# Optimization experiments

Measured on AMD Instinct MI355X. Metric: run time of the kernel, lower is better.

## Reference

```python
import jax, jax.numpy as jnp
import numpy as np


def _conv(x, w, b, stride, pad):
    # x: [N,C,H,W], w: [O,I,kh,kw]
    y = jax.lax.conv_general_dilated(
        x, w, (stride, stride), [(pad, pad), (pad, pad)],
        dimension_numbers=('NCHW', 'OIHW', 'NCHW'))
    return y + b[None, :, None, None]


def _block(x, w1, b1, w2, b2, stride):
    # BasicBlock with BN folded: conv3x3 -> relu -> conv3x3
    h = jax.nn.relu(_conv(x, w1, b1, stride, 1))
    return _conv(h, w2, b2, 1, 1)


def setup_inputs() -> dict:
    key = jax.random.key(0)
    keys = iter(jax.random.split(key, 64))

    def rn(shape):
        fan_in = int(np.prod(shape[1:])) if len(shape) > 1 else shape[0]
        return jax.random.normal(next(keys), shape, jnp.float32) * (1.0 / np.sqrt(fan_in))

    d = {}
    d['inputs'] = jax.random.normal(next(keys), (128, 3, 64, 64), jnp.float32)
    d['probs'] = jax.random.uniform(next(keys), (128, 15), jnp.float32)
    d['seed_w'] = rn((64, 3, 3, 3))
    d['seed_b'] = jnp.zeros((64,), jnp.float32)
    specs = [(64, 64), (64, 128), (128, 256)]  # (cin, cout) per group
    for g, (ci, co) in enumerate(specs):
        d[f'g{g}_ds_w'] = rn((co, ci, 1, 1))
        d[f'g{g}_ds_b'] = jnp.zeros((co,), jnp.float32)
        d[f'g{g}_b0_w1'] = rn((co, ci, 3, 3))
        d[f'g{g}_b0_b1'] = jnp.zeros((co,), jnp.float32)
        d[f'g{g}_b0_w2'] = rn((co, co, 3, 3))
        d[f'g{g}_b0_b2'] = jnp.zeros((co,), jnp.float32)
        d[f'g{g}_r_w1'] = rn((4, co, co, 3, 3))
        d[f'g{g}_r_b1'] = jnp.zeros((4, co), jnp.float32)
        d[f'g{g}_r_w2'] = rn((4, co, co, 3, 3))
        d[f'g{g}_r_b2'] = jnp.zeros((4, co), jnp.float32)
    d['fc_w'] = rn((1000, 256))
    d['fc_b'] = jnp.zeros((1000,), jnp.float32)
    return d


def reference(inputs, probs, seed_w, seed_b,
              g0_ds_w, g0_ds_b, g0_b0_w1, g0_b0_b1, g0_b0_w2, g0_b0_b2,
              g0_r_w1, g0_r_b1, g0_r_w2, g0_r_b2,
              g1_ds_w, g1_ds_b, g1_b0_w1, g1_b0_b1, g1_b0_w2, g1_b0_b2,
              g1_r_w1, g1_r_b1, g1_r_w2, g1_r_b2,
              g2_ds_w, g2_ds_b, g2_b0_w1, g2_b0_b1, g2_b0_w2, g2_b0_b2,
              g2_r_w1, g2_r_b1, g2_r_w2, g2_r_b2,
              fc_w, fc_b):
    # policy[k, n] in {0,1}: hard-threshold of agent probs at 0.5 (forward_real)
    policy = jnp.where(probs < 0.5, 0.0, 1.0).astype(inputs.dtype).T  # [15, B]
    x = jax.nn.relu(_conv(inputs, seed_w, seed_b, 1, 1))
    groups = [
        (g0_ds_w, g0_ds_b, g0_b0_w1, g0_b0_b1, g0_b0_w2, g0_b0_b2, g0_r_w1, g0_r_b1, g0_r_w2, g0_r_b2, 1),
        (g1_ds_w, g1_ds_b, g1_b0_w1, g1_b0_b1, g1_b0_w2, g1_b0_b2, g1_r_w1, g1_r_b1, g1_r_w2, g1_r_b2, 2),
        (g2_ds_w, g2_ds_b, g2_b0_w1, g2_b0_b1, g2_b0_w2, g2_b0_b2, g2_r_w1, g2_r_b1, g2_r_w2, g2_r_b2, 2),
    ]
    idx = 0
    for (ds_w, ds_b, b0_w1, b0_b1, b0_w2, b0_b2, r_w1, r_b1, r_w2, r_b2, s) in groups:
        # first block of the group: strided, with 1x1 downsample residual
        residual = _conv(x, ds_w, ds_b, s, 0)
        fx = _block(x, b0_w1, b0_b1, b0_w2, b0_b2, s)
        m = policy[idx][:, None, None, None]
        idx += 1
        x = m * jax.nn.relu(residual + fx) + (1.0 - m) * residual
        # remaining 4 identity-residual blocks
        for j in range(4):
            residual = x
            fx = _block(x, r_w1[j], r_b1[j], r_w2[j], r_b2[j], 1)
            m = policy[idx][:, None, None, None]
            idx += 1
            x = m * jax.nn.relu(residual + fx) + (1.0 - m) * residual
    pooled = x.mean(axis=(2, 3))  # global average pool [B, 256]
    return pooled @ fc_w.T + fc_b
```

## Files before the change

### kernel.cpp

```cpp
#include <hip/hip_runtime.h>

using bf = unsigned short;
typedef __attribute__((ext_vector_type(8))) short short8v;
typedef __attribute__((ext_vector_type(4))) float f32x4;
typedef __attribute__((ext_vector_type(4))) unsigned int u32x4;
typedef __attribute__((ext_vector_type(2))) unsigned int u32x2;

__device__ __forceinline__ float bf2f(bf u) { return __uint_as_float(((unsigned)u) << 16); }
__device__ __forceinline__ bf f2bf(float f) {
    unsigned x = __float_as_uint(f);
    x += 0x7fffu + ((x >> 16) & 1u);
    return (bf)(x >> 16);
}

__device__ __forceinline__ void gload16(const bf* g, bf* l) {
    __builtin_amdgcn_global_load_lds(
        (const __attribute__((address_space(1))) void*)g,
        (__attribute__((address_space(3))) void*)l, 16, 0, 0);
}

template <int CI, int CC, int RS, int STRIDE, bool RELU, int CMB, int TH, int TW, int W>
__global__ __launch_bounds__(256, 3) void conv_mfma(
    const bf* __restrict__ X, const bf* __restrict__ Wp,
    const float* __restrict__ bias, bf* __restrict__ Y,
    const bf* __restrict__ res, const float* __restrict__ probs,
    const bf* __restrict__ zpage, int kidx, int Co) {
    constexpr int PAD = (RS == 3) ? 1 : 0;
    constexpr int IN_ROWS = (TH - 1) * STRIDE + RS;
    constexpr int IN_COLS = (TW - 1) * STRIDE + RS;
    constexpr int NG = CC / 8;
    constexpr int HIN = W * STRIDE;
    constexpr int RSRS = RS * RS;
    constexpr int NCH = CI / CC;
    constexpr bool DIRECT = (RS == 1);
    constexpr int TG = IN_ROWS * IN_COLS * NG;
    constexpr int NITER = (TG + 255) / 256;
    constexpr int NPX = TH * TW;
    constexpr int NF = NPX / 32;
    constexpr int TPR = W / TW;
    constexpr int KSH = (STRIDE == 2) ? 1 : 0;

    __shared__ bf sX[DIRECT ? 8 : IN_ROWS * IN_COLS * CC];

    const int tid = threadIdx.x;
    const int n = blockIdx.z;
    const int coBase = blockIdx.y << 6;
    const int bx = blockIdx.x;
    const int tr0 = (bx / TPR) * TH;
    const int tc0 = (bx % TPR) * TW;

    bool active = true;
    if (kidx >= 0) active = (probs[n * 15 + kidx] >= 0.5f);
    if (!active) return;

    const int lane = tid & 63;
    const int wid = tid >> 6;
    const int l15 = lane & 15;
    const int lq = lane >> 4;
    const int wm = wid >> 1;
    const int wn = wid & 1;

    f32x4 acc[2][NF] = {};
    int prow[NF], pcol[NF];
#pragma unroll
    for (int nf = 0; nf < NF; ++nf) {
        int p = wn * (NPX / 2) + nf * 16 + l15;
        prow[nf] = p / TW;
        pcol[nf] = p % TW;
    }

    const bf* Xn = X + (size_t)n * HIN * HIN * CI;

    if constexpr (DIRECT) {
#pragma unroll
        for (int ch = 0; ch < NCH; ++ch) {
#pragma unroll
            for (int kk = 0; kk < CC / 32; ++kk) {
                short8v a[2], b[NF];
#pragma unroll
                for (int mf = 0; mf < 2; ++mf) {
                    int co = coBase + wm * 32 + mf * 16 + l15;
                    a[mf] = *reinterpret_cast<const short8v*>(
                        Wp + ((size_t)ch * Co + co) * CC + kk * 32 + lq * 8);
                }
#pragma unroll
                for (int nf = 0; nf < NF; ++nf) {
                    b[nf] = *reinterpret_cast<const short8v*>(
                        Xn + ((size_t)((tr0 + prow[nf]) * STRIDE) * HIN +
                              (tc0 + pcol[nf]) * STRIDE) * CI + ch * CC + kk * 32 + lq * 8);
                }
#pragma unroll
                for (int mf = 0; mf < 2; ++mf)
#pragma unroll
                    for (int nf = 0; nf < NF; ++nf)
                        acc[mf][nf] = __builtin_amdgcn_mfma_f32_16x16x32_bf16(
                            a[mf], b[nf], acc[mf][nf], 0, 0, 0);
            }
        }
    } else {
        for (int ch = 0; ch < NCH; ++ch) {
            if (ch) __syncthreads();
#pragma unroll
            for (int i = 0; i < NITER; ++i) {
                int g = tid + i * 256;
                if (TG % 256 == 0 || g < TG) {
                    int ir = g / (IN_COLS * NG);
                    int rem = g - ir * (IN_COLS * NG);
                    int ic = rem / NG;
                    int gc = rem - ic * NG;
                    int in_r = tr0 * STRIDE - PAD + ir;
                    int in_c = tc0 * STRIDE - PAD + ic;
                    int gsrc = gc ^ ((ic >> KSH) & (NG - 1));
                    const bf* src = zpage;
                    if ((unsigned)in_r < (unsigned)HIN && (unsigned)in_c < (unsigned)HIN)
                        src = Xn + ((size_t)in_r * HIN + in_c) * CI + ch * CC + gsrc * 8;
                    gload16(src, &sX[(size_t)g * 8]);
                }
            }
            __syncthreads();

            if constexpr (CC >= 32) {
#pragma unroll
                for (int j = 0; j < RSRS; ++j) {
                    const int dh = j / RS;
                    const int dw = j % RS;
#pragma unroll
                    for (int kk = 0; kk < CC / 32; ++kk) {
                        short8v a[2], b[NF];
#pragma unroll
                        for (int mf = 0; mf < 2; ++mf) {
                            int co = coBase + wm * 32 + mf * 16 + l15;
                            a[mf] = *reinterpret_cast<const short8v*>(
                                Wp + (((size_t)(ch * RSRS + j) * Co + co) * CC + kk * 32 + lq * 8));
                        }
#pragma unroll
                        for (int nf = 0; nf < NF; ++nf) {
                            int ir = prow[nf] * STRIDE + dh;
                            int ic = pcol[nf] * STRIDE + dw;
                            int gk = (kk * 4 + lq) ^ ((ic >> KSH) & (NG - 1));
                            b[nf] = *reinterpret_cast<const short8v*>(
                                &sX[((ir * IN_COLS + ic) * NG + gk) * 8]);
                        }
#pragma unroll
                        for (int mf = 0; mf < 2; ++mf)
#pragma unroll
                            for (int nf = 0; nf < NF; ++nf)
                                acc[mf][nf] = __builtin_amdgcn_mfma_f32_16x16x32_bf16(
                                    a[mf], b[nf], acc[mf][nf], 0, 0, 0);
                    }
                }
            } else {
#pragma unroll
                for (int kt = 0; kt < 3; ++kt) {
                    int j = kt * 4 + lq;
                    int jj = (j < 9) ? j : 0;
                    int dh = jj / 3, dw = jj % 3;
                    short8v a[2], b[NF];
#pragma unroll
                    for (int mf = 0; mf < 2; ++mf) {
                        int co = coBase + wm * 32 + mf * 16 + l15;
                        a[mf] = *reinterpret_cast<const short8v*>(Wp + ((size_t)j * Co + co) * 8);
                    }
#pragma unroll
                    for (int nf = 0; nf < NF; ++nf) {
                        int ir = prow[nf] + dh;
                        int ic = pcol[nf] + dw;
                        b[nf] = *reinterpret_cast<const short8v*>(&sX[(ir * IN_COLS + ic) * 8]);
                    }
#pragma unroll
                    for (int mf = 0; mf < 2; ++mf)
#pragma unroll
                        for (int nf = 0; nf < NF; ++nf)
                            acc[mf][nf] = __builtin_amdgcn_mfma_f32_16x16x32_bf16(
                                a[mf], b[nf], acc[mf][nf], 0, 0, 0);
                }
            }
        }
    }

#pragma unroll
    for (int mf = 0; mf < 2; ++mf) {
        int co0 = coBase + wm * 32 + mf * 16 + lq * 4;
        float4 b4 = *reinterpret_cast<const float4*>(bias + co0);
        float bb[4] = {b4.x, b4.y, b4.z, b4.w};
#pragma unroll
        for (int nf = 0; nf < NF; ++nf) {
            size_t off = ((size_t)n * W * W + (size_t)(tr0 + prow[nf]) * W + tc0 + pcol[nf]) * Co + co0;
            float v[4];
#pragma unroll
            for (int i = 0; i < 4; ++i) v[i] = acc[mf][nf][i] + bb[i];
            if constexpr (CMB >= 1) {
                u32x2 r2 = *reinterpret_cast<const u32x2*>(res + off);
                bf rr[4] = {(bf)(r2[0] & 0xffff), (bf)(r2[0] >> 16),
                            (bf)(r2[1] & 0xffff), (bf)(r2[1] >> 16)};
#pragma unroll
                for (int i = 0; i < 4; ++i) v[i] = fmaxf(v[i] + bf2f(rr[i]), 0.f);
            }
            if constexpr (RELU) {
#pragma unroll
                for (int i = 0; i < 4; ++i) v[i] = fmaxf(v[i], 0.f);
            }
            unsigned lo = (unsigned)f2bf(v[0]) | ((unsigned)f2bf(v[1]) << 16);
            unsigned hi = (unsigned)f2bf(v[2]) | ((unsigned)f2bf(v[3]) << 16);
            u32x2 o2 = {lo, hi};
            *reinterpret_cast<u32x2*>(Y + off) = o2;
        }
    }
}

#define NSEG 34
struct Seg {
    const float* src;
    bf* dst;
    int Co, Ci, RSRS, CC, JPAD, blk0;
};
struct SegArgs {
    Seg s[NSEG];
};
__global__ void repack_all(SegArgs A) {
    int b = blockIdx.x;
    int lo = 0;
#pragma unroll 1
    for (int i = 1; i < NSEG; ++i)
        if (A.s[i].blk0 <= b) lo = i;
    Seg sg = A.s[lo];
    int NCH_ = (sg.Ci + sg.CC - 1) / sg.CC;
    size_t total8 = ((size_t)NCH_ * sg.JPAD * sg.Co * sg.CC) >> 3;
    size_t i8 = (size_t)(b - sg.blk0) * 256 + threadIdx.x;
    if (i8 >= total8) return;
    size_t e = i8 * 8;
    int cw = (int)(e % sg.CC);
    int co = (int)((e / sg.CC) % sg.Co);
    int j = (int)((e / ((size_t)sg.CC * sg.Co)) % sg.JPAD);
    int ch = (int)(e / ((size_t)sg.CC * sg.Co * sg.JPAD));
    bf tmp[8];
#pragma unroll
    for (int k = 0; k < 8; ++k) {
        int ci = ch * sg.CC + cw + k;
        float v = 0.f;
        if (ci < sg.Ci && j < sg.RSRS) v = sg.src[((size_t)co * sg.Ci + ci) * sg.RSRS + j];
        tmp[k] = f2bf(v);
    }
    u32x4 o;
#pragma unroll
    for (int k = 0; k < 4; ++k) o[k] = (unsigned)tmp[2 * k] | ((unsigned)tmp[2 * k + 1] << 16);
    *reinterpret_cast<u32x4*>(sg.dst + e) = o;
}

__global__ void cvt_in(const float* __restrict__ in, bf* __restrict__ out) {
    size_t idx = (size_t)blockIdx.x * 256 + threadIdx.x;
    int c = (int)(idx & 7);
    size_t pix = idx >> 3;
    int w = (int)(pix & 63);
    int h = (int)((pix >> 6) & 63);
    int n = (int)(pix >> 12);
    float v = 0.f;
    if (c < 3) v = in[(((size_t)n * 3 + c) * 64 + h) * 64 + w];
    out[idx] = f2bf(v);
}

__global__ void zero_k(bf* p) {
    u32x4 z = {0, 0, 0, 0};
    *reinterpret_cast<u32x4*>(p + (size_t)threadIdx.x * 8) = z;
}

__global__ void pool_k(const bf* __restrict__ X, float* __restrict__ pooled) {
    __shared__ float red[8][256];
    int n = blockIdx.x;
    int g = threadIdx.x & 31;
    int slice = threadIdx.x >> 5;
    float acc[8] = {};
    for (int p = slice * 32; p < slice * 32 + 32; ++p) {
        u32x4 v = *reinterpret_cast<const u32x4*>(X + ((size_t)n * 256 + p) * 256 + g * 8);
#pragma unroll
        for (int i = 0; i < 4; ++i) {
            acc[2 * i] += bf2f((bf)(v[i] & 0xffff));
            acc[2 * i + 1] += bf2f((bf)(v[i] >> 16));
        }
    }
#pragma unroll
    for (int i = 0; i < 8; ++i) red[slice][g * 8 + i] = acc[i];
    __syncthreads();
    if (slice == 0) {
#pragma unroll
        for (int i = 0; i < 8; ++i) {
            float s = 0.f;
#pragma unroll
            for (int ss = 0; ss < 8; ++ss) s += red[ss][g * 8 + i];
            pooled[n * 256 + g * 8 + i] = s * (1.f / 256.f);
        }
    }
}

__global__ void fc_k(const float* __restrict__ pooled, const float* __restrict__ fw,
                     const float* __restrict__ fb, float* __restrict__ out) {
    __shared__ float sp[256];
    int n = blockIdx.x;
    sp[threadIdx.x] = pooled[n * 256 + threadIdx.x];
    __syncthreads();
    for (int o = threadIdx.x; o < 1000; o += 256) {
        float acc = fb[o];
        for (int k = 0; k < 256; ++k) acc += sp[k] * fw[(size_t)o * 256 + k];
        out[(size_t)n * 1000 + o] = acc;
    }
}

template <int CIN, int COUT, int S, int TH, int TW, int W, int CC1>
static void run_group(hipStream_t st, bf* X, bf* H, bf* OUT, const bf* zp,
                      bf* wp_ds, const float* ds_b, bf* wp_w1, const float* b1,
                      bf* wp_w2, const float* b2, bf* const* wp_rw1, const float* rb1,
                      bf* const* wp_rw2, const float* rb2, const float* probs_c,
                      int kbase, int NB) {
    dim3 grid((W / TH) * (W / TW), COUT / 64, NB);
    conv_mfma<CIN, 64, 1, S, false, 0, TH, TW, W><<<grid, 256, 0, st>>>(
        X, wp_ds, ds_b, OUT, nullptr, nullptr, zp, -1, COUT);
    conv_mfma<CIN, CC1, 3, S, true, 0, TH, TW, W><<<grid, 256, 0, st>>>(
        X, wp_w1, b1, H, nullptr, probs_c, zp, kbase, COUT);
    conv_mfma<COUT, 64, 3, 1, false, 2, TH, TW, W><<<grid, 256, 0, st>>>(
        H, wp_w2, b2, OUT, OUT, probs_c, zp, kbase, COUT);
    for (int j = 0; j < 4; ++j) {
        conv_mfma<COUT, 64, 3, 1, true, 0, TH, TW, W><<<grid, 256, 0, st>>>(
            OUT, wp_rw1[j], rb1 + j * COUT, H, nullptr, probs_c, zp, kbase + 1 + j, COUT);
        conv_mfma<COUT, 64, 3, 1, false, 2, TH, TW, W><<<grid, 256, 0, st>>>(
            H, wp_rw2[j], rb2 + j * COUT, OUT, OUT, probs_c, zp, kbase + 1 + j, COUT);
    }
}

extern "C" void kernel_launch(void* const* d_in, const int* in_sizes, int n_in,
                              void* d_out, int out_size, void* d_ws, size_t ws_size,
                              hipStream_t stream) {
    (void)in_sizes; (void)n_in; (void)out_size;
    const float* input = (const float*)d_in[0];
    const float* probs = (const float*)d_in[1];
    const float* seed_w = (const float*)d_in[2];
    const float* seed_b = (const float*)d_in[3];
    const float* fc_w = (const float*)d_in[34];
    const float* fc_b = (const float*)d_in[35];

    char* pw = (char*)d_ws;
    auto alloc = [&](size_t bytes) -> void* {
        void* r = (void*)pw;
        pw += ((bytes + 255) & ~(size_t)255);
        return r;
    };

    bf* xin = (bf*)alloc(128ull * 64 * 64 * 8 * 2);
    float* pooled = (float*)alloc(128 * 256 * 4);
    bf* zpage = (bf*)alloc(256);

    SegArgs sa;
    int nseg = 0;
    int blkAcc = 0;
    auto pack = [&](const float* w, int Co_, int Ci_, int RSRS_, int CC_, int JPAD_) -> bf* {
        int NCH_ = (Ci_ + CC_ - 1) / CC_;
        size_t total = (size_t)NCH_ * JPAD_ * Co_ * CC_;
        bf* wp = (bf*)alloc(total * 2);
        sa.s[nseg] = {w, wp, Co_, Ci_, RSRS_, CC_, JPAD_, blkAcc};
        blkAcc += (int)(((total >> 3) + 255) / 256);
        ++nseg;
        return wp;
    };

    zero_k<<<dim3(1), 16, 0, stream>>>(zpage);
    cvt_in<<<dim3(16384), 256, 0, stream>>>(input, xin);

    bf* wpSeed = pack(seed_w, 64, 3, 9, 8, 12);
    const int cis[3] = {64, 64, 128};
    const int cos[3] = {64, 128, 256};
    const int cc1s[3] = {64, 32, 32};
    bf* wp_ds[3];
    bf* wp_w1[3];
    bf* wp_w2[3];
    bf* wp_rw1[3][4];
    bf* wp_rw2[3][4];
    const float *ds_b[3], *b1[3], *b2[3], *rb1[3], *rb2[3];
    for (int g = 0; g < 3; ++g) {
        int base = 4 + g * 10;
        const float* dsw = (const float*)d_in[base + 0];
        ds_b[g] = (const float*)d_in[base + 1];
        const float* w1 = (const float*)d_in[base + 2];
        b1[g] = (const float*)d_in[base + 3];
        const float* w2 = (const float*)d_in[base + 4];
        b2[g] = (const float*)d_in[base + 5];
        const float* rw1 = (const float*)d_in[base + 6];
        rb1[g] = (const float*)d_in[base + 7];
        const float* rw2 = (const float*)d_in[base + 8];
        rb2[g] = (const float*)d_in[base + 9];
        int Ci = cis[g], Co = cos[g];
        wp_ds[g] = pack(dsw, Co, Ci, 1, 64, 1);
        wp_w1[g] = pack(w1, Co, Ci, 9, cc1s[g], 9);
        wp_w2[g] = pack(w2, Co, Co, 9, 64, 9);
        for (int j = 0; j < 4; ++j) {
            wp_rw1[g][j] = pack(rw1 + (size_t)j * Co * Co * 9, Co, Co, 9, 64, 9);
            wp_rw2[g][j] = pack(rw2 + (size_t)j * Co * Co * 9, Co, Co, 9, 64, 9);
        }
    }
    for (int i = nseg; i < NSEG; ++i) sa.s[i] = {nullptr, nullptr, 1, 1, 1, 1, 1, 0x7fffffff};
    repack_all<<<dim3(blkAcc), 256, 0, stream>>>(sa);

    size_t used = (size_t)(pw - (char*)d_ws);
    size_t avail = (ws_size > used) ? (ws_size - used) : 0;
    const size_t PER_IMG = 64ull * 64 * 64 * 2;
    int NB = 128;
    while (NB > 8 && (size_t)3 * NB * PER_IMG + 4096 > avail) NB >>= 1;

    bf* A = (bf*)alloc((size_t)NB * PER_IMG);
    bf* Bb = (bf*)alloc((size_t)NB * PER_IMG);
    bf* C = (bf*)alloc((size_t)NB * PER_IMG);

    for (int n0 = 0; n0 < 128; n0 += NB) {
        const float* pc = probs + (size_t)n0 * 15;
        conv_mfma<8, 8, 3, 1, true, 0, 8, 16, 64><<<dim3(32, 1, NB), 256, 0, stream>>>(
            xin + (size_t)n0 * 64 * 64 * 8, wpSeed, seed_b, A, nullptr, nullptr, zpage, -1, 64);

        run_group<64, 64, 1, 8, 16, 64, 64>(stream, A, Bb, C, zpage,
                                            wp_ds[0], ds_b[0], wp_w1[0], b1[0],
                                            wp_w2[0], b2[0], wp_rw1[0], rb1[0],
                                            wp_rw2[0], rb2[0], pc, 0, NB);
        run_group<64, 128, 2, 8, 16, 32, 32>(stream, C, Bb, A, zpage,
                                             wp_ds[1], ds_b[1], wp_w1[1], b1[1],
                                             wp_w2[1], b2[1], wp_rw1[1], rb1[1],
                                             wp_rw2[1], rb2[1], pc, 5, NB);
        run_group<128, 256, 2, 8, 8, 16, 32>(stream, A, Bb, C, zpage,
                                             wp_ds[2], ds_b[2], wp_w1[2], b1[2],
                                             wp_w2[2], b2[2], wp_rw1[2], rb1[2],
                                             wp_rw2[2], rb2[2], pc, 10, NB);

        pool_k<<<dim3(NB), 256, 0, stream>>>(C, pooled + (size_t)n0 * 256);
    }

    fc_k<<<dim3(128), 256, 0, stream>>>(pooled, fc_w, fc_b, (float*)d_out);
}
```

Baseline: 2.360 ms.

## Double-buffer LDS staging with 32-channel chunks and register-held weights

Switches all 3x3 convs to 32-channel input chunks and double-buffers the LDS tile, so the next chunk's global-to-LDS copy overlaps the MFMA compute on the current one. All nine taps of weights for a chunk are preloaded into registers before use. Tile shapes are also split per conv type: first-block convs and residual convs get separate tile sizes, and group 2 switches to larger tiles. This adds register pressure (18 short8v for weights) and more LDS, which may reduce occupancy under launch_bounds(256,3).

```diff
diff --git a/kernel.cpp b/kernel.cpp
--- a/kernel.cpp
+++ b/kernel.cpp
@@ -35,12 +35,15 @@
     constexpr bool DIRECT = (RS == 1);
     constexpr int TG = IN_ROWS * IN_COLS * NG;
     constexpr int NITER = (TG + 255) / 256;
+    constexpr int TGP = NITER * 256;
+    constexpr int BUFE = TGP * 8;
     constexpr int NPX = TH * TW;
     constexpr int NF = NPX / 32;
     constexpr int TPR = W / TW;
     constexpr int KSH = (STRIDE == 2) ? 1 : 0;
-
-    __shared__ bf sX[DIRECT ? 8 : IN_ROWS * IN_COLS * CC];
+    constexpr bool PIPE = (!DIRECT) && (CC == 32) && (NCH > 1);
+
+    __shared__ bf sX[DIRECT ? 8 : (PIPE ? 2 * BUFE : BUFE)];
 
     const int tid = threadIdx.x;
     const int n = blockIdx.z;
@@ -97,84 +100,116 @@
                             a[mf], b[nf], acc[mf][nf], 0, 0, 0);
             }
         }
-    } else {
-        for (int ch = 0; ch < NCH; ++ch) {
-            if (ch) __syncthreads();
+    } else if constexpr (CC == 32) {
+        short8v wl[RSRS][2];
+
+        auto wload = [&](int ch) {
+#pragma unroll
+            for (int j = 0; j < RSRS; ++j)
+#pragma unroll
+                for (int mf = 0; mf < 2; ++mf) {
+                    int co = coBase + wm * 32 + mf * 16 + l15;
+                    wl[j][mf] = *reinterpret_cast<const short8v*>(
+                        Wp + (((size_t)(ch * RSRS + j) * Co + co) * CC + lq * 8));
+                }
+        };
+
+        auto stage = [&](int ch, bf* buf) {
 #pragma unroll
             for (int i = 0; i < NITER; ++i) {
                 int g = tid + i * 256;
-                if (TG % 256 == 0 || g < TG) {
-                    int ir = g / (IN_COLS * NG);
-                    int rem = g - ir * (IN_COLS * NG);
-                    int ic = rem / NG;
-                    int gc = rem - ic * NG;
-                    int in_r = tr0 * STRIDE - PAD + ir;
-                    int in_c = tc0 * STRIDE - PAD + ic;
-                    int gsrc = gc ^ ((ic >> KSH) & (NG - 1));
-                    const bf* src = zpage;
-                    if ((unsigned)in_r < (unsigned)HIN && (unsigned)in_c < (unsigned)HIN)
-                        src = Xn + ((size_t)in_r * HIN + in_c) * CI + ch * CC + gsrc * 8;
-                    gload16(src, &sX[(size_t)g * 8]);
+                int ir = g / (IN_COLS * NG);
+                int rem = g - ir * (IN_COLS * NG);
+                int ic = rem / NG;
+                int gc = rem - ic * NG;
+                int in_r = tr0 * STRIDE - PAD + ir;
+                int in_c = tc0 * STRIDE - PAD + ic;
+                int gsrc = gc ^ ((ic >> KSH) & (NG - 1));
+                const bf* src = zpage;
+                if (g < TG && (unsigned)in_r < (unsigned)HIN && (unsigned)in_c < (unsigned)HIN)
+                    src = Xn + ((size_t)in_r * HIN + in_c) * CI + ch * CC + gsrc * 8;
+                gload16(src, &buf[(size_t)g * 8]);
+            }
+        };
+
+        auto compute = [&](const bf* buf) {
+#pragma unroll
+            for (int j = 0; j < RSRS; ++j) {
+                const int dh = j / RS;
+                const int dw = j % RS;
+                short8v b[NF];
+#pragma unroll
+                for (int nf = 0; nf < NF; ++nf) {
+                    int ir = prow[nf] * STRIDE + dh;
+                    int ic = pcol[nf] * STRIDE + dw;
+                    int gk = lq ^ ((ic >> KSH) & (NG - 1));
+                    b[nf] = *reinterpret_cast<const short8v*>(
+                        &buf[((ir * IN_COLS + ic) * NG + gk) * 8]);
                 }
-            }
-            __syncthreads();
-
-            if constexpr (CC >= 32) {
-#pragma unroll
-                for (int j = 0; j < RSRS; ++j) {
-                    const int dh = j / RS;
-                    const int dw = j % RS;
-#pragma unroll
-                    for (int kk = 0; kk < CC / 32; ++kk) {
-                        short8v a[2], b[NF];
-#pragma unroll
-                        for (int mf = 0; mf < 2; ++mf) {
-                            int co = coBase + wm * 32 + mf * 16 + l15;
-                            a[mf] = *reinterpret_cast<const short8v*>(
-                                Wp + (((size_t)(ch * RSRS + j) * Co + co) * CC + kk * 32 + lq * 8));
-                        }
-#pragma unroll
-                        for (int nf = 0; nf < NF; ++nf) {
-                            int ir = prow[nf] * STRIDE + dh;
-                            int ic = pcol[nf] * STRIDE + dw;
-                            int gk = (kk * 4 + lq) ^ ((ic >> KSH) & (NG - 1));
-                            b[nf] = *reinterpret_cast<const short8v*>(
-                                &sX[((ir * IN_COLS + ic) * NG + gk) * 8]);
-                        }
-#pragma unroll
-                        for (int mf = 0; mf < 2; ++mf)
-#pragma unroll
-                            for (int nf = 0; nf < NF; ++nf)
-                                acc[mf][nf] = __builtin_amdgcn_mfma_f32_16x16x32_bf16(
-                                    a[mf], b[nf], acc[mf][nf], 0, 0, 0);
-                    }
-                }
-            } else {
-#pragma unroll
-                for (int kt = 0; kt < 3; ++kt) {
-                    int j = kt * 4 + lq;
-                    int jj = (j < 9) ? j : 0;
-                    int dh = jj / 3, dw = jj % 3;
-                    short8v a[2], b[NF];
-#pragma unroll
-                    for (int mf = 0; mf < 2; ++mf) {
-                        int co = coBase + wm * 32 + mf * 16 + l15;
-                        a[mf] = *reinterpret_cast<const short8v*>(Wp + ((size_t)j * Co + co) * 8);
-                    }
-#pragma unroll
-                    for (int nf = 0; nf < NF; ++nf) {
-                        int ir = prow[nf] + dh;
-                        int ic = pcol[nf] + dw;
-                        b[nf] = *reinterpret_cast<const short8v*>(&sX[(ir * IN_COLS + ic) * 8]);
-                    }
-#pragma unroll
-                    for (int mf = 0; mf < 2; ++mf)
-#pragma unroll
-                        for (int nf = 0; nf < NF; ++nf)
-                            acc[mf][nf] = __builtin_amdgcn_mfma_f32_16x16x32_bf16(
-                                a[mf], b[nf], acc[mf][nf], 0, 0, 0);
-                }
-            }
+#pragma unroll
+                for (int mf = 0; mf < 2; ++mf)
+#pragma unroll
+                    for (int nf = 0; nf < NF; ++nf)
+                        acc[mf][nf] = __builtin_amdgcn_mfma_f32_16x16x32_bf16(
+                            wl[j][mf], b[nf], acc[mf][nf], 0, 0, 0);
+            }
+        };
+
+        wload(0);
+        __builtin_amdgcn_sched_barrier(0);
+        stage(0, sX);
+        __syncthreads();
+#pragma unroll 1
+        for (int ch = 0; ch < NCH; ++ch) {
+            const bf* cur = sX + (size_t)(PIPE ? (ch & 1) : 0) * BUFE;
+            bf* nxt = sX + (size_t)(PIPE ? ((ch + 1) & 1) : 0) * BUFE;
+            if (ch + 1 < NCH) stage(ch + 1, nxt);
+            __builtin_amdgcn_sched_barrier(0);
+            compute(cur);
+            if (ch + 1 < NCH) {
+                wload(ch + 1);
+                __syncthreads();
+            }
+        }
+    } else {
+        stage_seed:;
+#pragma unroll
+        for (int i = 0; i < NITER; ++i) {
+            int g = tid + i * 256;
+            int ir = g / (IN_COLS * NG);
+            int rem = g - ir * (IN_COLS * NG);
+            int ic = rem / NG;
+            int in_r = tr0 - PAD + ir;
+            int in_c = tc0 - PAD + ic;
+            const bf* src = zpage;
+            if (g < TG && (unsigned)in_r < (unsigned)HIN && (unsigned)in_c < (unsigned)HIN)
+                src = Xn + ((size_t)in_r * HIN + in_c) * CI;
+            gload16(src, &sX[(size_t)g * 8]);
+        }
+        __syncthreads();
+#pragma unroll
+        for (int kt = 0; kt < 3; ++kt) {
+            int j = kt * 4 + lq;
+            int jj = (j < 9) ? j : 0;
+            int dh = jj / 3, dw = jj % 3;
+            short8v a[2], b[NF];
+#pragma unroll
+            for (int mf = 0; mf < 2; ++mf) {
+                int co = coBase + wm * 32 + mf * 16 + l15;
+                a[mf] = *reinterpret_cast<const short8v*>(Wp + ((size_t)j * Co + co) * 8);
+            }
+#pragma unroll
+            for (int nf = 0; nf < NF; ++nf) {
+                int ir = prow[nf] + dh;
+                int ic = pcol[nf] + dw;
+                b[nf] = *reinterpret_cast<const short8v*>(&sX[(ir * IN_COLS + ic) * 8]);
+            }
+#pragma unroll
+            for (int mf = 0; mf < 2; ++mf)
+#pragma unroll
+                for (int nf = 0; nf < NF; ++nf)
+                    acc[mf][nf] = __builtin_amdgcn_mfma_f32_16x16x32_bf16(
+                        a[mf], b[nf], acc[mf][nf], 0, 0, 0);
         }
     }
 
@@ -305,23 +340,24 @@
     }
 }
 
-template <int CIN, int COUT, int S, int TH, int TW, int W, int CC1>
+template <int CIN, int COUT, int S, int TH1, int TW1, int TH2, int TW2, int W>
 static void run_group(hipStream_t st, bf* X, bf* H, bf* OUT, const bf* zp,
                       bf* wp_ds, const float* ds_b, bf* wp_w1, const float* b1,
                       bf* wp_w2, const float* b2, bf* const* wp_rw1, const float* rb1,
                       bf* const* wp_rw2, const float* rb2, const float* probs_c,
                       int kbase, int NB) {
-    dim3 grid((W / TH) * (W / TW), COUT / 64, NB);
-    conv_mfma<CIN, 64, 1, S, false, 0, TH, TW, W><<<grid, 256, 0, st>>>(
+    dim3 grid1((W / TH1) * (W / TW1), COUT / 64, NB);
+    dim3 grid2((W / TH2) * (W / TW2), COUT / 64, NB);
+    conv_mfma<CIN, 64, 1, S, false, 0, TH2, TW2, W><<<grid2, 256, 0, st>>>(
         X, wp_ds, ds_b, OUT, nullptr, nullptr, zp, -1, COUT);
-    conv_mfma<CIN, CC1, 3, S, true, 0, TH, TW, W><<<grid, 256, 0, st>>>(
+    conv_mfma<CIN, 32, 3, S, true, 0, TH2, TW2, W><<<grid2, 256, 0, st>>>(
         X, wp_w1, b1, H, nullptr, probs_c, zp, kbase, COUT);
-    conv_mfma<COUT, 64, 3, 1, false, 2, TH, TW, W><<<grid, 256, 0, st>>>(
+    conv_mfma<COUT, 32, 3, 1, false, 2, TH1, TW1, W><<<grid1, 256, 0, st>>>(
         H, wp_w2, b2, OUT, OUT, probs_c, zp, kbase, COUT);
     for (int j = 0; j < 4; ++j) {
-        conv_mfma<COUT, 64, 3, 1, true, 0, TH, TW, W><<<grid, 256, 0, st>>>(
+        conv_mfma<COUT, 32, 3, 1, true, 0, TH1, TW1, W><<<grid1, 256, 0, st>>>(
             OUT, wp_rw1[j], rb1 + j * COUT, H, nullptr, probs_c, zp, kbase + 1 + j, COUT);
-        conv_mfma<COUT, 64, 3, 1, false, 2, TH, TW, W><<<grid, 256, 0, st>>>(
+        conv_mfma<COUT, 32, 3, 1, false, 2, TH1, TW1, W><<<grid1, 256, 0, st>>>(
             H, wp_rw2[j], rb2 + j * COUT, OUT, OUT, probs_c, zp, kbase + 1 + j, COUT);
     }
 }
@@ -367,7 +403,6 @@
     bf* wpSeed = pack(seed_w, 64, 3, 9, 8, 12);
     const int cis[3] = {64, 64, 128};
     const int cos[3] = {64, 128, 256};
-    const int cc1s[3] = {64, 32, 32};
     bf* wp_ds[3];
     bf* wp_w1[3];
     bf* wp_w2[3];
@@ -388,11 +423,11 @@
         rb2[g] = (const float*)d_in[base + 9];
         int Ci = cis[g], Co = cos[g];
         wp_ds[g] = pack(dsw, Co, Ci, 1, 64, 1);
-        wp_w1[g] = pack(w1, Co, Ci, 9, cc1s[g], 9);
-        wp_w2[g] = pack(w2, Co, Co, 9, 64, 9);
+        wp_w1[g] = pack(w1, Co, Ci, 9, 32, 9);
+        wp_w2[g] = pack(w2, Co, Co, 9, 32, 9);
         for (int j = 0; j < 4; ++j) {
-            wp_rw1[g][j] = pack(rw1 + (size_t)j * Co * Co * 9, Co, Co, 9, 64, 9);
-            wp_rw2[g][j] = pack(rw2 + (size_t)j * Co * Co * 9, Co, Co, 9, 64, 9);
+            wp_rw1[g][j] = pack(rw1 + (size_t)j * Co * Co * 9, Co, Co, 9, 32, 9);
+            wp_rw2[g][j] = pack(rw2 + (size_t)j * Co * Co * 9, Co, Co, 9, 32, 9);
         }
     }
     for (int i = nseg; i < NSEG; ++i) sa.s[i] = {nullptr, nullptr, 1, 1, 1, 1, 1, 0x7fffffff};
@@ -413,18 +448,18 @@
         conv_mfma<8, 8, 3, 1, true, 0, 8, 16, 64><<<dim3(32, 1, NB), 256, 0, stream>>>(
             xin + (size_t)n0 * 64 * 64 * 8, wpSeed, seed_b, A, nullptr, nullptr, zpage, -1, 64);
 
-        run_group<64, 64, 1, 8, 16, 64, 64>(stream, A, Bb, C, zpage,
-                                            wp_ds[0], ds_b[0], wp_w1[0], b1[0],
-                                            wp_w2[0], b2[0], wp_rw1[0], rb1[0],
-                                            wp_rw2[0], rb2[0], pc, 0, NB);
-        run_group<64, 128, 2, 8, 16, 32, 32>(stream, C, Bb, A, zpage,
-                                             wp_ds[1], ds_b[1], wp_w1[1], b1[1],
-                                             wp_w2[1], b2[1], wp_rw1[1], rb1[1],
-                                             wp_rw2[1], rb2[1], pc, 5, NB);
-        run_group<128, 256, 2, 8, 8, 16, 32>(stream, A, Bb, C, zpage,
-                                             wp_ds[2], ds_b[2], wp_w1[2], b1[2],
-                                             wp_w2[2], b2[2], wp_rw1[2], rb1[2],
-                                             wp_rw2[2], rb2[2], pc, 10, NB);
+        run_group<64, 64, 1, 8, 16, 8, 16, 64>(stream, A, Bb, C, zpage,
+                                               wp_ds[0], ds_b[0], wp_w1[0], b1[0],
+                                               wp_w2[0], b2[0], wp_rw1[0], rb1[0],
+                                               wp_rw2[0], rb2[0], pc, 0, NB);
+        run_group<64, 128, 2, 8, 16, 8, 8, 32>(stream, C, Bb, A, zpage,
+                                               wp_ds[1], ds_b[1], wp_w1[1], b1[1],
+                                               wp_w2[1], b2[1], wp_rw1[1], rb1[1],
+                                               wp_rw2[1], rb2[1], pc, 5, NB);
+        run_group<128, 256, 2, 8, 16, 8, 8, 16>(stream, A, Bb, C, zpage,
+                                                wp_ds[2], ds_b[2], wp_w1[2], b1[2],
+                                                wp_w2[2], b2[2], wp_rw1[2], rb1[2],
+                                                wp_rw2[2], rb2[2], pc, 10, NB);
 
         pool_k<<<dim3(NB), 256, 0, stream>>>(C, pooled + (size_t)n0 * 256);
     }
```

Result: slower. 3.096 ms (+31.2%).

## Fuse downsample 1x1 conv into first block conv, seed input cast, and pool+fc

Applied to the files above, without the earlier changes.

The 1x1 strided downsample conv is now computed inside the first 3x3 conv of each group, reusing the staged input tile (the center tap). Inactive images run only the downsample path. The fp32-to-bf16 input conversion kernel is folded into the seed conv's tile load, and average pooling is merged with the FC layer. This removes separate launches and redundant reads of activations, at the cost of extra registers for a second accumulator set in the fused kernel.

```diff
diff --git a/kernel.cpp b/kernel.cpp
--- a/kernel.cpp
+++ b/kernel.cpp
@@ -19,28 +19,27 @@
         (__attribute__((address_space(3))) void*)l, 16, 0, 0);
 }
 
-template <int CI, int CC, int RS, int STRIDE, bool RELU, int CMB, int TH, int TW, int W>
+template <int CI, int CC, int STRIDE, bool SEED, bool DS, bool RELU, int CMB,
+          int TH, int TW, int W>
 __global__ __launch_bounds__(256, 3) void conv_mfma(
-    const bf* __restrict__ X, const bf* __restrict__ Wp,
-    const float* __restrict__ bias, bf* __restrict__ Y,
+    const bf* __restrict__ X, const float* __restrict__ Xf,
+    const bf* __restrict__ Wp, const bf* __restrict__ Wds,
+    const float* __restrict__ bias, const float* __restrict__ dsb,
+    bf* __restrict__ Y, bf* __restrict__ Yds,
     const bf* __restrict__ res, const float* __restrict__ probs,
     const bf* __restrict__ zpage, int kidx, int Co) {
-    constexpr int PAD = (RS == 3) ? 1 : 0;
-    constexpr int IN_ROWS = (TH - 1) * STRIDE + RS;
-    constexpr int IN_COLS = (TW - 1) * STRIDE + RS;
+    constexpr int IN_ROWS = (TH - 1) * STRIDE + 3;
+    constexpr int IN_COLS = (TW - 1) * STRIDE + 3;
     constexpr int NG = CC / 8;
     constexpr int HIN = W * STRIDE;
-    constexpr int RSRS = RS * RS;
     constexpr int NCH = CI / CC;
-    constexpr bool DIRECT = (RS == 1);
     constexpr int TG = IN_ROWS * IN_COLS * NG;
     constexpr int NITER = (TG + 255) / 256;
-    constexpr int NPX = TH * TW;
-    constexpr int NF = NPX / 32;
+    constexpr int NF = (TH * TW) / 32;
     constexpr int TPR = W / TW;
     constexpr int KSH = (STRIDE == 2) ? 1 : 0;
 
-    __shared__ bf sX[DIRECT ? 8 : IN_ROWS * IN_COLS * CC];
+    __shared__ bf sX[SEED ? TG * 8 : NITER * 256 * 8];
 
     const int tid = threadIdx.x;
     const int n = blockIdx.z;
@@ -51,7 +50,7 @@
 
     bool active = true;
     if (kidx >= 0) active = (probs[n * 15 + kidx] >= 0.5f);
-    if (!active) return;
+    if (!active && !DS) return;
 
     const int lane = tid & 63;
     const int wid = tid >> 6;
@@ -61,33 +60,70 @@
     const int wn = wid & 1;
 
     f32x4 acc[2][NF] = {};
+    f32x4 accds[DS ? 2 : 1][DS ? NF : 1] = {};
     int prow[NF], pcol[NF];
 #pragma unroll
     for (int nf = 0; nf < NF; ++nf) {
-        int p = wn * (NPX / 2) + nf * 16 + l15;
+        int p = wn * (TH * TW / 2) + nf * 16 + l15;
         prow[nf] = p / TW;
         pcol[nf] = p % TW;
     }
 
     const bf* Xn = X + (size_t)n * HIN * HIN * CI;
 
-    if constexpr (DIRECT) {
-#pragma unroll
-        for (int ch = 0; ch < NCH; ++ch) {
-#pragma unroll
-            for (int kk = 0; kk < CC / 32; ++kk) {
+    for (int ch = 0; ch < NCH; ++ch) {
+        if (ch) __syncthreads();
+        if constexpr (SEED) {
+            const float* Xfn = Xf + (size_t)n * 3 * HIN * HIN;
+            if (tid < TG) {
+                int ir = tid / IN_COLS;
+                int ic = tid % IN_COLS;
+                int in_r = tr0 - 1 + ir;
+                int in_c = tc0 - 1 + ic;
+                u32x4 u = {0, 0, 0, 0};
+                if ((unsigned)in_r < (unsigned)HIN && (unsigned)in_c < (unsigned)HIN) {
+                    const float* p = Xfn + (size_t)in_r * HIN + in_c;
+                    u[0] = (unsigned)f2bf(p[0]) | ((unsigned)f2bf(p[HIN * HIN]) << 16);
+                    u[1] = (unsigned)f2bf(p[2 * HIN * HIN]);
+                }
+                *reinterpret_cast<u32x4*>(&sX[(size_t)tid * 8]) = u;
+            }
+        } else {
+#pragma unroll
+            for (int i = 0; i < NITER; ++i) {
+                int g = tid + i * 256;
+                int ir = g / (IN_COLS * NG);
+                int rem = g - ir * (IN_COLS * NG);
+                int ic = rem / NG;
+                int gc = rem - ic * NG;
+                int in_r = tr0 * STRIDE - 1 + ir;
+                int in_c = tc0 * STRIDE - 1 + ic;
+                int gsrc = gc ^ ((ic >> KSH) & (NG - 1));
+                const bf* src = zpage;
+                if (g < TG && (unsigned)in_r < (unsigned)HIN && (unsigned)in_c < (unsigned)HIN)
+                    src = Xn + ((size_t)in_r * HIN + in_c) * CI + ch * CC + gsrc * 8;
+                gload16(src, &sX[(size_t)g * 8]);
+            }
+        }
+        __syncthreads();
+
+        if constexpr (SEED) {
+#pragma unroll
+            for (int kt = 0; kt < 3; ++kt) {
+                int j = kt * 4 + lq;
+                int jj = (j < 9) ? j : 0;
+                int dh = jj / 3, dw = jj % 3;
                 short8v a[2], b[NF];
 #pragma unroll
                 for (int mf = 0; mf < 2; ++mf) {
                     int co = coBase + wm * 32 + mf * 16 + l15;
-                    a[mf] = *reinterpret_cast<const short8v*>(
-                        Wp + ((size_t)ch * Co + co) * CC + kk * 32 + lq * 8);
+                    a[mf] = *reinterpret_cast<const short8v*>(Wp + ((size_t)j * Co + co) * 8);
                 }
 #pragma unroll
                 for (int nf = 0; nf < NF; ++nf) {
-                    b[nf] = *reinterpret_cast<const short8v*>(
-                        Xn + ((size_t)((tr0 + prow[nf]) * STRIDE) * HIN +
-                              (tc0 + pcol[nf]) * STRIDE) * CI + ch * CC + kk * 32 + lq * 8);
+                    int ir = prow[nf] + dh;
+                    int ic = pcol[nf] + dw;
+                    b[nf] = *reinterpret_cast<const short8v*>(&sX[(ir * IN_COLS + ic) * 8]);
                 }
 #pragma unroll
                 for (int mf = 0; mf < 2; ++mf)
@@ -96,76 +132,27 @@
                         acc[mf][nf] = __builtin_amdgcn_mfma_f32_16x16x32_bf16(
                             a[mf], b[nf], acc[mf][nf], 0, 0, 0);
             }
-        }
-    } else {
-        for (int ch = 0; ch < NCH; ++ch) {
-            if (ch) __syncthreads();
-#pragma unroll
-            for (int i = 0; i < NITER; ++i) {
-                int g = tid + i * 256;
-                if (TG % 256 == 0 || g < TG) {
-                    int ir = g / (IN_COLS * NG);
-                    int rem = g - ir * (IN_COLS * NG);
-                    int ic = rem / NG;
-                    int gc = rem - ic * NG;
-                    int in_r = tr0 * STRIDE - PAD + ir;
-                    int in_c = tc0 * STRIDE - PAD + ic;
-                    int gsrc = gc ^ ((ic >> KSH) & (NG - 1));
-                    const bf* src = zpage;
-                    if ((unsigned)in_r < (unsigned)HIN && (unsigned)in_c < (unsigned)HIN)
-                        src = Xn + ((size_t)in_r * HIN + in_c) * CI + ch * CC + gsrc * 8;
-                    gload16(src, &sX[(size_t)g * 8]);
-                }
-            }
-            __syncthreads();
-
-            if constexpr (CC >= 32) {
-#pragma unroll
-                for (int j = 0; j < RSRS; ++j) {
-                    const int dh = j / RS;
-                    const int dw = j % RS;
-#pragma unroll
-                    for (int kk = 0; kk < CC / 32; ++kk) {
-                        short8v a[2], b[NF];
-#pragma unroll
-                        for (int mf = 0; mf < 2; ++mf) {
-                            int co = coBase + wm * 32 + mf * 16 + l15;
-                            a[mf] = *reinterpret_cast<const short8v*>(
-                                Wp + (((size_t)(ch * RSRS + j) * Co + co) * CC + kk * 32 + lq * 8));
-                        }
-#pragma unroll
-                        for (int nf = 0; nf < NF; ++nf) {
-                            int ir = prow[nf] * STRIDE + dh;
-                            int ic = pcol[nf] * STRIDE + dw;
-                            int gk = (kk * 4 + lq) ^ ((ic >> KSH) & (NG - 1));
-                            b[nf] = *reinterpret_cast<const short8v*>(
-                                &sX[((ir * IN_COLS + ic) * NG + gk) * 8]);
-                        }
-#pragma unroll
-                        for (int mf = 0; mf < 2; ++mf)
-#pragma unroll
-                            for (int nf = 0; nf < NF; ++nf)
-                                acc[mf][nf] = __builtin_amdgcn_mfma_f32_16x16x32_bf16(
-                                    a[mf], b[nf], acc[mf][nf], 0, 0, 0);
-                    }
-                }
-            } else {
-#pragma unroll
-                for (int kt = 0; kt < 3; ++kt) {
-                    int j = kt * 4 + lq;
-                    int jj = (j < 9) ? j : 0;
-                    int dh = jj / 3, dw = jj % 3;
+        } else if (active) {
+#pragma unroll
+            for (int j = 0; j < 9; ++j) {
+                const int dh = j / 3;
+                const int dw = j % 3;
+#pragma unroll
+                for (int kk = 0; kk < CC / 32; ++kk) {
                     short8v a[2], b[NF];
 #pragma unroll
                     for (int mf = 0; mf < 2; ++mf) {
                         int co = coBase + wm * 32 + mf * 16 + l15;
-                        a[mf] = *reinterpret_cast<const short8v*>(Wp + ((size_t)j * Co + co) * 8);
+                        a[mf] = *reinterpret_cast<const short8v*>(
+                            Wp + (((size_t)(ch * 9 + j) * Co + co) * CC + kk * 32 + lq * 8));
                     }
 #pragma unroll
                     for (int nf = 0; nf < NF; ++nf) {
-                        int ir = prow[nf] + dh;
-                        int ic = pcol[nf] + dw;
-                        b[nf] = *reinterpret_cast<const short8v*>(&sX[(ir * IN_COLS + ic) * 8]);
+                        int ir = prow[nf] * STRIDE + dh;
+                        int ic = pcol[nf] * STRIDE + dw;
+                        int gk = (kk * 4 + lq) ^ ((ic >> KSH) & (NG - 1));
+                        b[nf] = *reinterpret_cast<const short8v*>(
+                            &sX[((ir * IN_COLS + ic) * NG + gk) * 8]);
                     }
 #pragma unroll
                     for (int mf = 0; mf < 2; ++mf)
@@ -173,7 +160,49 @@
                         for (int nf = 0; nf < NF; ++nf)
                             acc[mf][nf] = __builtin_amdgcn_mfma_f32_16x16x32_bf16(
                                 a[mf], b[nf], acc[mf][nf], 0, 0, 0);
-                }
+                    if constexpr (DS) {
+                        if (j == 4) {
+                            short8v ads[2];
+#pragma unroll
+                            for (int mf = 0; mf < 2; ++mf) {
+                                int co = coBase + wm * 32 + mf * 16 + l15;
+                                ads[mf] = *reinterpret_cast<const short8v*>(
+                                    Wds + ((size_t)ch * Co + co) * CC + kk * 32 + lq * 8);
+                            }
+#pragma unroll
+                            for (int mf = 0; mf < 2; ++mf)
+#pragma unroll
+                                for (int nf = 0; nf < NF; ++nf)
+                                    accds[mf][nf] = __builtin_amdgcn_mfma_f32_16x16x32_bf16(
+                                        ads[mf], b[nf], accds[mf][nf], 0, 0, 0);
+                        }
+                    }
+                }
+            }
+        } else if constexpr (DS) {
+#pragma unroll
+            for (int kk = 0; kk < CC / 32; ++kk) {
+                short8v ads[2], b[NF];
+#pragma unroll
+                for (int mf = 0; mf < 2; ++mf) {
+                    int co = coBase + wm * 32 + mf * 16 + l15;
+                    ads[mf] = *reinterpret_cast<const short8v*>(
+                        Wds + ((size_t)ch * Co + co) * CC + kk * 32 + lq * 8);
+                }
+#pragma unroll
+                for (int nf = 0; nf < NF; ++nf) {
+                    int ir = prow[nf] * STRIDE + 1;
+                    int ic = pcol[nf] * STRIDE + 1;
+                    int gk = (kk * 4 + lq) ^ ((ic >> KSH) & (NG - 1));
+                    b[nf] = *reinterpret_cast<const short8v*>(
+                        &sX[((ir * IN_COLS + ic) * NG + gk) * 8]);
+                }
+#pragma unroll
+                for (int mf = 0; mf < 2; ++mf)
+#pragma unroll
+                    for (int nf = 0; nf < NF; ++nf)
+                        accds[mf][nf] = __builtin_amdgcn_mfma_f32_16x16x32_bf16(
+                            ads[mf], b[nf], accds[mf][nf], 0, 0, 0);
             }
         }
     }
@@ -181,29 +210,41 @@
 #pragma unroll
     for (int mf = 0; mf < 2; ++mf) {
         int co0 = coBase + wm * 32 + mf * 16 + lq * 4;
-        float4 b4 = *reinterpret_cast<const float4*>(bias + co0);
-        float bb[4] = {b4.x, b4.y, b4.z, b4.w};
 #pragma unroll
         for (int nf = 0; nf < NF; ++nf) {
             size_t off = ((size_t)n * W * W + (size_t)(tr0 + prow[nf]) * W + tc0 + pcol[nf]) * Co + co0;
-            float v[4];
-#pragma unroll
-            for (int i = 0; i < 4; ++i) v[i] = acc[mf][nf][i] + bb[i];
-            if constexpr (CMB >= 1) {
-                u32x2 r2 = *reinterpret_cast<const u32x2*>(res + off);
-                bf rr[4] = {(bf)(r2[0] & 0xffff), (bf)(r2[0] >> 16),
-                            (bf)(r2[1] & 0xffff), (bf)(r2[1] >> 16)};
-#pragma unroll
-                for (int i = 0; i < 4; ++i) v[i] = fmaxf(v[i] + bf2f(rr[i]), 0.f);
-            }
-            if constexpr (RELU) {
-#pragma unroll
-                for (int i = 0; i < 4; ++i) v[i] = fmaxf(v[i], 0.f);
-            }
-            unsigned lo = (unsigned)f2bf(v[0]) | ((unsigned)f2bf(v[1]) << 16);
-            unsigned hi = (unsigned)f2bf(v[2]) | ((unsigned)f2bf(v[3]) << 16);
-            u32x2 o2 = {lo, hi};
-            *reinterpret_cast<u32x2*>(Y + off) = o2;
+            if constexpr (DS) {
+                float4 d4 = *reinterpret_cast<const float4*>(dsb + co0);
+                float v[4];
+#pragma unroll
+                for (int i = 0; i < 4; ++i)
+                    v[i] = accds[mf][nf][i] + ((const float*)&d4)[i];
+                unsigned lo = (unsigned)f2bf(v[0]) | ((unsigned)f2bf(v[1]) << 16);
+                unsigned hi = (unsigned)f2bf(v[2]) | ((unsigned)f2bf(v[3]) << 16);
+                u32x2 o2 = {lo, hi};
+                *reinterpret_cast<u32x2*>(Yds + off) = o2;
+            }
+            if (active) {
+                float4 b4 = *reinterpret_cast<const float4*>(bias + co0);
+                float v[4];
+#pragma unroll
+                for (int i = 0; i < 4; ++i) v[i] = acc[mf][nf][i] + ((const float*)&b4)[i];
+                if constexpr (CMB >= 1) {
+                    u32x2 r2 = *reinterpret_cast<const u32x2*>(res + off);
+                    bf rr[4] = {(bf)(r2[0] & 0xffff), (bf)(r2[0] >> 16),
+                                (bf)(r2[1] & 0xffff), (bf)(r2[1] >> 16)};
+#pragma unroll
+                    for (int i = 0; i < 4; ++i) v[i] = fmaxf(v[i] + bf2f(rr[i]), 0.f);
+                }
+                if constexpr (RELU) {
+#pragma unroll
+                    for (int i = 0; i < 4; ++i) v[i] = fmaxf(v[i], 0.f);
+                }
+                unsigned lo = (unsigned)f2bf(v[0]) | ((unsigned)f2bf(v[1]) << 16);
+                unsigned hi = (unsigned)f2bf(v[2]) | ((unsigned)f2bf(v[3]) << 16);
+                u32x2 o2 = {lo, hi};
+                *reinterpret_cast<u32x2*>(Y + off) = o2;
+            }
         }
     }
 }
@@ -247,25 +288,15 @@
     *reinterpret_cast<u32x4*>(sg.dst + e) = o;
 }
 
-__global__ void cvt_in(const float* __restrict__ in, bf* __restrict__ out) {
-    size_t idx = (size_t)blockIdx.x * 256 + threadIdx.x;
-    int c = (int)(idx & 7);
-    size_t pix = idx >> 3;
-    int w = (int)(pix & 63);
-    int h = (int)((pix >> 6) & 63);
-    int n = (int)(pix >> 12);
-    float v = 0.f;
-    if (c < 3) v = in[(((size_t)n * 3 + c) * 64 + h) * 64 + w];
-    out[idx] = f2bf(v);
-}
-
 __global__ void zero_k(bf* p) {
     u32x4 z = {0, 0, 0, 0};
     *reinterpret_cast<u32x4*>(p + (size_t)threadIdx.x * 8) = z;
 }
 
-__global__ void pool_k(const bf* __restrict__ X, float* __restrict__ pooled) {
+__global__ void poolfc_k(const bf* __restrict__ X, const float* __restrict__ fw,
+                         const float* __restrict__ fb, float* __restrict__ out) {
     __shared__ float red[8][256];
+    __shared__ float sp[256];
     int n = blockIdx.x;
     int g = threadIdx.x & 31;
     int slice = threadIdx.x >> 5;
@@ -287,42 +318,35 @@
             float s = 0.f;
 #pragma unroll
             for (int ss = 0; ss < 8; ++ss) s += red[ss][g * 8 + i];
-            pooled[n * 256 + g * 8 + i] = s * (1.f / 256.f);
-        }
-    }
-}
-
-__global__ void fc_k(const float* __restrict__ pooled, const float* __restrict__ fw,
-                     const float* __restrict__ fb, float* __restrict__ out) {
-    __shared__ float sp[256];
-    int n = blockIdx.x;
-    sp[threadIdx.x] = pooled[n * 256 + threadIdx.x];
+            sp[g * 8 + i] = s * (1.f / 256.f);
+        }
+    }
     __syncthreads();
     for (int o = threadIdx.x; o < 1000; o += 256) {
-        float acc = fb[o];
-        for (int k = 0; k < 256; ++k) acc += sp[k] * fw[(size_t)o * 256 + k];
-        out[(size_t)n * 1000 + o] = acc;
-    }
-}
-
-template <int CIN, int COUT, int S, int TH, int TW, int W, int CC1>
+        float a = fb[o];
+        for (int k = 0; k < 256; ++k) a += sp[k] * fw[(size_t)o * 256 + k];
+        out[(size_t)n * 1000 + o] = a;
+    }
+}
+
+template <int CIN, int COUT, int S, int CC1, int W>
 static void run_group(hipStream_t st, bf* X, bf* H, bf* OUT, const bf* zp,
                       bf* wp_ds, const float* ds_b, bf* wp_w1, const float* b1,
                       bf* wp_w2, const float* b2, bf* const* wp_rw1, const float* rb1,
                       bf* const* wp_rw2, const float* rb2, const float* probs_c,
                       int kbase, int NB) {
-    dim3 grid((W / TH) * (W / TW), COUT / 64, NB);
-    conv_mfma<CIN, 64, 1, S, false, 0, TH, TW, W><<<grid, 256, 0, st>>>(
-        X, wp_ds, ds_b, OUT, nullptr, nullptr, zp, -1, COUT);
-    conv_mfma<CIN, CC1, 3, S, true, 0, TH, TW, W><<<grid, 256, 0, st>>>(
-        X, wp_w1, b1, H, nullptr, probs_c, zp, kbase, COUT);
-    conv_mfma<COUT, 64, 3, 1, false, 2, TH, TW, W><<<grid, 256, 0, st>>>(
-        H, wp_w2, b2, OUT, OUT, probs_c, zp, kbase, COUT);
+    dim3 grid((W / 8) * (W / 16), COUT / 64, NB);
+    conv_mfma<CIN, CC1, S, false, true, true, 0, 8, 16, W><<<grid, 256, 0, st>>>(
+        X, nullptr, wp_w1, wp_ds, b1, ds_b, H, OUT, nullptr, probs_c, zp, kbase, COUT);
+    conv_mfma<COUT, 64, 1, false, false, false, 2, 8, 16, W><<<grid, 256, 0, st>>>(
+        H, nullptr, wp_w2, nullptr, b2, nullptr, OUT, nullptr, OUT, probs_c, zp, kbase, COUT);
     for (int j = 0; j < 4; ++j) {
-        conv_mfma<COUT, 64, 3, 1, true, 0, TH, TW, W><<<grid, 256, 0, st>>>(
-            OUT, wp_rw1[j], rb1 + j * COUT, H, nullptr, probs_c, zp, kbase + 1 + j, COUT);
-        conv_mfma<COUT, 64, 3, 1, false, 2, TH, TW, W><<<grid, 256, 0, st>>>(
-            H, wp_rw2[j], rb2 + j * COUT, OUT, OUT, probs_c, zp, kbase + 1 + j, COUT);
+        conv_mfma<COUT, 64, 1, false, false, true, 0, 8, 16, W><<<grid, 256, 0, st>>>(
+            OUT, nullptr, wp_rw1[j], nullptr, rb1 + j * COUT, nullptr, H, nullptr,
+            nullptr, probs_c, zp, kbase + 1 + j, COUT);
+        conv_mfma<COUT, 64, 1, false, false, false, 2, 8, 16, W><<<grid, 256, 0, st>>>(
+            H, nullptr, wp_rw2[j], nullptr, rb2 + j * COUT, nullptr, OUT, nullptr,
+            OUT, probs_c, zp, kbase + 1 + j, COUT);
     }
 }
 
@@ -344,8 +368,6 @@
         return r;
     };
 
-    bf* xin = (bf*)alloc(128ull * 64 * 64 * 8 * 2);
-    float* pooled = (float*)alloc(128 * 256 * 4);
     bf* zpage = (bf*)alloc(256);
 
     SegArgs sa;
@@ -362,7 +384,6 @@
     };
 
     zero_k<<<dim3(1), 16, 0, stream>>>(zpage);
-    cvt_in<<<dim3(16384), 256, 0, stream>>>(input, xin);
 
     bf* wpSeed = pack(seed_w, 64, 3, 9, 8, 12);
     const int cis[3] = {64, 64, 128};
@@ -387,7 +408,7 @@
         const float* rw2 = (const float*)d_in[base + 8];
         rb2[g] = (const float*)d_in[base + 9];
         int Ci = cis[g], Co = cos[g];
-        wp_ds[g] = pack(dsw, Co, Ci, 1, 64, 1);
+        wp_ds[g] = pack(dsw, Co, Ci, 1, cc1s[g], 1);
         wp_w1[g] = pack(w1, Co, Ci, 9, cc1s[g], 9);
         wp_w2[g] = pack(w2, Co, Co, 9, 64, 9);
         for (int j = 0; j < 4; ++j) {
@@ -410,24 +431,21 @@
 
     for (int n0 = 0; n0 < 128; n0 += NB) {
         const float* pc = probs + (size_t)n0 * 15;
-        conv_mfma<8, 8, 3, 1, true, 0, 8, 16, 64><<<dim3(32, 1, NB), 256, 0, stream>>>(
-            xin + (size_t)n0 * 64 * 64 * 8, wpSeed, seed_b, A, nullptr, nullptr, zpage, -1, 64);
-
-        run_group<64, 64, 1, 8, 16, 64, 64>(stream, A, Bb, C, zpage,
-                                            wp_ds[0], ds_b[0], wp_w1[0], b1[0],
-                                            wp_w2[0], b2[0], wp_rw1[0], rb1[0],
-                                            wp_rw2[0], rb2[0], pc, 0, NB);
-        run_group<64, 128, 2, 8, 16, 32, 32>(stream, C, Bb, A, zpage,
-                                             wp_ds[1], ds_b[1], wp_w1[1], b1[1],
-                                             wp_w2[1], b2[1], wp_rw1[1], rb1[1],
-                                             wp_rw2[1], rb2[1], pc, 5, NB);
-        run_group<128, 256, 2, 8, 8, 16, 32>(stream, A, Bb, C, zpage,
-                                             wp_ds[2], ds_b[2], wp_w1[2], b1[2],
-                                             wp_w2[2], b2[2], wp_rw1[2], rb1[2],
-                                             wp_rw2[2], rb2[2], pc, 10, NB);
-
-        pool_k<<<dim3(NB), 256, 0, stream>>>(C, pooled + (size_t)n0 * 256);
-    }
-
-    fc_k<<<dim3(128), 256, 0, stream>>>(pooled, fc_w, fc_b, (float*)d_out);
-}
+        conv_mfma<8, 8, 1, true, false, true, 0, 8, 16, 64><<<dim3(32, 1, NB), 256, 0, stream>>>(
+            nullptr, input + (size_t)n0 * 3 * 4096, wpSeed, nullptr, seed_b, nullptr,
+            A, nullptr, nullptr, nullptr, zpage, -1, 64);
+
+        run_group<64, 64, 1, 64, 64>(stream, A, Bb, C, zpage,
+                                     wp_ds[0], ds_b[0], wp_w1[0], b1[0], wp_w2[0], b2[0],
+                                     wp_rw1[0], rb1[0], wp_rw2[0], rb2[0], pc, 0, NB);
+        run_group<64, 128, 2, 32, 32>(stream, C, Bb, A, zpage,
+                                      wp_ds[1], ds_b[1], wp_w1[1], b1[1], wp_w2[1], b2[1],
+                                      wp_rw1[1], rb1[1], wp_rw2[1], rb2[1], pc, 5, NB);
+        run_group<128, 256, 2, 32, 16>(stream, A, Bb, C, zpage,
+                                       wp_ds[2], ds_b[2], wp_w1[2], b1[2], wp_w2[2], b2[2],
+                                       wp_rw1[2], rb1[2], wp_rw2[2], rb2[2], pc, 10, NB);
+
+        poolfc_k<<<dim3(NB), 256, 0, stream>>>(C, fc_w, fc_b,
+                                               (float*)d_out + (size_t)n0 * 1000);
+    }
+}
```

Measured after the change: 2.182 ms. 1.08x faster.
